# Kernel optimization log

Hardware: AMD Instinct MI355X
Metric: run time of the kernel (lower is better)

The kernel has to match this reference:

```python
import jax, jax.numpy as jnp
import numpy as np
from jax import lax

FILTER_SIZE = 3
C_IN = 128
C_OUT = 256
PAD = 1
STRIDE = 1


def setup_inputs() -> dict:
    key = jax.random.key(0)
    k1, k2 = jax.random.split(key)
    prev_a = jax.random.normal(k1, (32, 56, 56, C_IN), dtype=jnp.float32)
    # filter_w initialized ~ N(0, 1) as in the original tf.random.normal
    filter_w = jax.random.normal(k2, (FILTER_SIZE, FILTER_SIZE, C_IN, C_OUT), dtype=jnp.float32)
    filter_b = jnp.zeros((1, 1, 1, C_OUT), dtype=jnp.float32)
    return {"prev_a": prev_a, "filter_w": filter_w, "filter_b": filter_b}


def reference(prev_a, filter_w, filter_b):
    # NHWC input, HWIO filter -> NHWC output; same math as the nested-loop conv:
    # z[i,h,w,c] = sum(prev_a_pad[i, h*s:h*s+f, w*s:w*s+f, :] * W[:,:,:,c]) + b[c]
    z = lax.conv_general_dilated(
        prev_a,
        filter_w,
        window_strides=(STRIDE, STRIDE),
        padding=[(PAD, PAD), (PAD, PAD)],
        dimension_numbers=("NHWC", "HWIO", "NHWC"),
    )
    z = z + filter_b  # bias broadcast over (m, H, W)
    return jax.nn.relu(z)
```

## Files before the change

### kernel.cpp

```cpp
#include <hip/hip_runtime.h>
#include <hip/hip_bf16.h>


#define NIMG 32
#define HH 56
#define WW 56
#define PH 58
#define PW 58
#define CIN 128
#define COUT 256
#define KTOT 1152
#define PAD_ELEMS (NIMG * PH * PW * CIN)

typedef __attribute__((ext_vector_type(8))) short bf16x8;
typedef __attribute__((ext_vector_type(4))) short s16x4;
typedef __attribute__((ext_vector_type(4))) float f32x4;

__device__ __forceinline__ short f2bf(float x) {
    union { __hip_bfloat16 b; short s; } u;
    u.b = __float2bfloat16(x);
    return u.s;
}

typedef const void __attribute__((address_space(1)))* gas1_t;
typedef void __attribute__((address_space(3)))* las3_t;
__device__ __forceinline__ void async16(short* lds, const short* g) {
    __builtin_amdgcn_global_load_lds((gas1_t)g, (las3_t)lds, 16, 0, 0);
}

__global__ __launch_bounds__(256) void pack_input(const float* __restrict__ in,
                                                  short* __restrict__ pad) {
    const int tid  = blockIdx.x * 256 + threadIdx.x;
    const int flat = tid * 8;
    const int c8   = flat & (CIN - 1);
    const int rest = flat >> 7;
    const int iw   = rest % PW;
    const int r2   = rest / PW;
    const int ih   = r2 % PH;
    const int img  = r2 / PH;
    bf16x8 v = (bf16x8)0;
    if (ih >= 1 && ih <= HH && iw >= 1 && iw <= WW) {
        const float* p = in + (((size_t)(img * HH + ih - 1) * WW + (iw - 1)) * CIN + c8);
        const float4 x0 = *(const float4*)p;
        const float4 x1 = *(const float4*)(p + 4);
        v.s0 = f2bf(x0.x); v.s1 = f2bf(x0.y); v.s2 = f2bf(x0.z); v.s3 = f2bf(x0.w);
        v.s4 = f2bf(x1.x); v.s5 = f2bf(x1.y); v.s6 = f2bf(x1.z); v.s7 = f2bf(x1.w);
    }
    *(bf16x8*)(pad + flat) = v;
}

__global__ __launch_bounds__(256) void pack_wgt(const float* __restrict__ w,
                                                short* __restrict__ wt) {
    __shared__ short tile[32][33];
    const int k0 = blockIdx.x * 32;
    const int n0 = blockIdx.y * 32;
    const int t  = threadIdx.x;
    {
        const int kl  = t >> 3;
        const int nl4 = (t & 7) * 4;
        const float4 x = *(const float4*)(w + (size_t)(k0 + kl) * COUT + n0 + nl4);
        tile[kl][nl4 + 0] = f2bf(x.x);
        tile[kl][nl4 + 1] = f2bf(x.y);
        tile[kl][nl4 + 2] = f2bf(x.z);
        tile[kl][nl4 + 3] = f2bf(x.w);
    }
    __syncthreads();
    {
        const int nl  = t >> 3;
        const int kl4 = (t & 7) * 4;
        s16x4 v;
        v.x = tile[kl4 + 0][nl];
        v.y = tile[kl4 + 1][nl];
        v.z = tile[kl4 + 2][nl];
        v.w = tile[kl4 + 3][nl];
        *(s16x4*)(wt + (size_t)(n0 + nl) * KTOT + k0 + kl4) = v;
    }
}

__global__ __launch_bounds__(256) void conv_mfma(const short* __restrict__ apad,
                                                 const short* __restrict__ bwt,
                                                 const float* __restrict__ bias,
                                                 float* __restrict__ out) {
    __shared__ short As[128 * 32];
    __shared__ short Bs[128 * 32];

    const int t  = threadIdx.x;
    const int l  = t & 63;
    const int w  = t >> 6;
    const int m0 = blockIdx.y * 128;
    const int n0 = blockIdx.x * 128;

    const int kchunk = t & 3;
    const int row0   = t >> 2;
    int abase[2], bbase[2];
#pragma unroll
    for (int j = 0; j < 2; ++j) {
        const int m   = m0 + row0 + j * 64;
        const int img = m / (HH * WW);
        const int rem = m - img * (HH * WW);
        const int oh  = rem / WW;
        const int ow  = rem - oh * WW;
        abase[j] = ((img * PH + oh) * PW + ow) * CIN + kchunk * 8;
        bbase[j] = (n0 + row0 + j * 64) * KTOT + kchunk * 8;
    }

    f32x4 acc[4][4];
#pragma unroll
    for (int i = 0; i < 4; ++i)
#pragma unroll
        for (int j = 0; j < 4; ++j) { f32x4 z = {0.f, 0.f, 0.f, 0.f}; acc[i][j] = z; }

    const int wm = w & 1;
    const int wn = w >> 1;
    const int fr = l & 15;
    const int fq = l >> 4;

    for (int kt = 0; kt < KTOT / 32; ++kt) {
        const int fhw  = kt >> 2;
        const int ci0  = (kt & 3) * 32;
        const int fh   = fhw / 3;
        const int fw   = fhw - fh * 3;
        const int aoff = (fh * PW + fw) * CIN + ci0;
        const int boff = kt * 32;

        __syncthreads();
#pragma unroll
        for (int j = 0; j < 2; ++j) {
            async16(As + (j * 256 + w * 64) * 8, apad + abase[j] + aoff);
            async16(Bs + (j * 256 + w * 64) * 8, bwt + bbase[j] + boff);
        }
        __syncthreads();

        bf16x8 af[4], bf[4];
#pragma unroll
        for (int i = 0; i < 4; ++i)
            af[i] = *(bf16x8*)&As[(wm * 64 + i * 16 + fr) * 32 + fq * 8];
#pragma unroll
        for (int j = 0; j < 4; ++j)
            bf[j] = *(bf16x8*)&Bs[(wn * 64 + j * 16 + fr) * 32 + fq * 8];
#pragma unroll
        for (int i = 0; i < 4; ++i)
#pragma unroll
            for (int j = 0; j < 4; ++j)
                acc[i][j] = __builtin_amdgcn_mfma_f32_16x16x32_bf16(af[i], bf[j], acc[i][j], 0, 0, 0);
    }

#pragma unroll
    for (int j = 0; j < 4; ++j) {
        const int n  = n0 + wn * 64 + j * 16 + fr;
        const float bj = bias[n];
#pragma unroll
        for (int i = 0; i < 4; ++i) {
            const int mrow = m0 + wm * 64 + i * 16 + fq * 4;
#pragma unroll
            for (int r = 0; r < 4; ++r) {
                const float v = acc[i][j][r] + bj;
                out[(size_t)(mrow + r) * COUT + n] = v > 0.f ? v : 0.f;
            }
        }
    }
}

extern "C" void kernel_launch(void* const* d_in, const int* in_sizes, int n_in,
                              void* d_out, int out_size, void* d_ws, size_t ws_size,
                              hipStream_t stream) {
    const float* in   = (const float*)d_in[0];
    const float* wgt  = (const float*)d_in[1];
    const float* bias = (const float*)d_in[2];
    float* out = (float*)d_out;

    short* pad = (short*)d_ws;
    short* wt  = (short*)d_ws + PAD_ELEMS;

    pack_input<<<PAD_ELEMS / 8 / 256, 256, 0, stream>>>(in, pad);
    pack_wgt<<<dim3(KTOT / 32, COUT / 32), 256, 0, stream>>>(wgt, wt);

    dim3 grid(COUT / 128, (NIMG * HH * WW) / 128);
    conv_mfma<<<grid, 256, 0, stream>>>(pad, wt, bias, out);
}
```

Before: 224.1 us.

## Double-buffer LDS tiles and XOR-swizzle the layout in the conv MFMA kernel

```diff
diff --git a/kernel.cpp b/kernel.cpp
--- a/kernel.cpp
+++ b/kernel.cpp
@@ -11,6 +11,9 @@
 #define COUT 256
 #define KTOT 1152
 #define PAD_ELEMS (NIMG * PH * PW * CIN)
+
+#define BK 32
+#define KITERS (KTOT / BK)
 
 typedef __attribute__((ext_vector_type(8))) short bf16x8;
 typedef __attribute__((ext_vector_type(4))) short s16x4;
@@ -81,8 +84,8 @@
                                                  const short* __restrict__ bwt,
                                                  const float* __restrict__ bias,
                                                  float* __restrict__ out) {
-    __shared__ short As[128 * 32];
-    __shared__ short Bs[128 * 32];
+    __shared__ short As0[128 * BK], As1[128 * BK];
+    __shared__ short Bs0[128 * BK], Bs1[128 * BK];
 
     const int t  = threadIdx.x;
     const int l  = t & 63;
@@ -90,18 +93,19 @@
     const int m0 = blockIdx.y * 128;
     const int n0 = blockIdx.x * 128;
 
-    const int kchunk = t & 3;
-    const int row0   = t >> 2;
+    const int Lc = (t & 7) ^ ((t >> 3) & 7);
+    const int kc = Lc & 3;
     int abase[2], bbase[2];
 #pragma unroll
     for (int j = 0; j < 2; ++j) {
-        const int m   = m0 + row0 + j * 64;
+        const int r   = 2 * (t >> 3) + (Lc >> 2) + j * 64;
+        const int m   = m0 + r;
         const int img = m / (HH * WW);
         const int rem = m - img * (HH * WW);
         const int oh  = rem / WW;
         const int ow  = rem - oh * WW;
-        abase[j] = ((img * PH + oh) * PW + ow) * CIN + kchunk * 8;
-        bbase[j] = (n0 + row0 + j * 64) * KTOT + kchunk * 8;
+        abase[j] = ((img * PH + oh) * PW + ow) * CIN + kc * 8;
+        bbase[j] = (n0 + r) * KTOT + kc * 8;
     }
 
     f32x4 acc[4][4];
@@ -115,34 +119,45 @@
     const int fr = l & 15;
     const int fq = l >> 4;
 
-    for (int kt = 0; kt < KTOT / 32; ++kt) {
-        const int fhw  = kt >> 2;
-        const int ci0  = (kt & 3) * 32;
-        const int fh   = fhw / 3;
-        const int fw   = fhw - fh * 3;
-        const int aoff = (fh * PW + fw) * CIN + ci0;
-        const int boff = kt * 32;
+#define STAGE(KT, AS, BS) do {                                              \
+        const int _fhw  = (KT) >> 2;                                        \
+        const int _fh   = _fhw / 3;                                         \
+        const int _fw   = _fhw - _fh * 3;                                   \
+        const int _aoff = (_fh * PW + _fw) * CIN + ((KT) & 3) * 32;         \
+        const int _boff = (KT) * BK;                                        \
+        _Pragma("unroll")                                                   \
+        for (int _j = 0; _j < 2; ++_j) {                                    \
+            async16((AS) + (_j * 256 + w * 64) * 8, apad + abase[_j] + _aoff); \
+            async16((BS) + (_j * 256 + w * 64) * 8, bwt + bbase[_j] + _boff); \
+        }                                                                   \
+    } while (0)
 
+#define FRAG(BASE, R) \
+    (*(const bf16x8*)((BASE) + (((R) >> 1) << 6) + \
+     (((((R) & 1) << 2) | fq) ^ (((R) >> 1) & 7)) * 8))
+
+#define COMPUTE(AS, BS) do {                                                \
+        bf16x8 _af[4], _bf[4];                                              \
+        _Pragma("unroll")                                                   \
+        for (int _i = 0; _i < 4; ++_i) _af[_i] = FRAG(AS, wm * 64 + _i * 16 + fr); \
+        _Pragma("unroll")                                                   \
+        for (int _j = 0; _j < 4; ++_j) _bf[_j] = FRAG(BS, wn * 64 + _j * 16 + fr); \
+        _Pragma("unroll")                                                   \
+        for (int _i = 0; _i < 4; ++_i)                                      \
+            _Pragma("unroll")                                               \
+            for (int _j = 0; _j < 4; ++_j)                                  \
+                acc[_i][_j] = __builtin_amdgcn_mfma_f32_16x16x32_bf16(      \
+                    _af[_i], _bf[_j], acc[_i][_j], 0, 0, 0);                \
+    } while (0)
+
+    STAGE(0, As0, Bs0);
+    for (int kt = 0; kt < KITERS; kt += 2) {
         __syncthreads();
-#pragma unroll
-        for (int j = 0; j < 2; ++j) {
-            async16(As + (j * 256 + w * 64) * 8, apad + abase[j] + aoff);
-            async16(Bs + (j * 256 + w * 64) * 8, bwt + bbase[j] + boff);
-        }
+        STAGE(kt + 1, As1, Bs1);
+        COMPUTE(As0, Bs0);
         __syncthreads();
-
-        bf16x8 af[4], bf[4];
-#pragma unroll
-        for (int i = 0; i < 4; ++i)
-            af[i] = *(bf16x8*)&As[(wm * 64 + i * 16 + fr) * 32 + fq * 8];
-#pragma unroll
-        for (int j = 0; j < 4; ++j)
-            bf[j] = *(bf16x8*)&Bs[(wn * 64 + j * 16 + fr) * 32 + fq * 8];
-#pragma unroll
-        for (int i = 0; i < 4; ++i)
-#pragma unroll
-            for (int j = 0; j < 4; ++j)
-                acc[i][j] = __builtin_amdgcn_mfma_f32_16x16x32_bf16(af[i], bf[j], acc[i][j], 0, 0, 0);
+        if (kt + 2 < KITERS) STAGE(kt + 2, As0, Bs0);
+        COMPUTE(As1, Bs1);
     }
 
 #pragma unroll
@@ -159,6 +174,9 @@
             }
         }
     }
+#undef STAGE
+#undef FRAG
+#undef COMPUTE
 }
 
 extern "C" void kernel_launch(void* const* d_in, const int* in_sizes, int n_in,
```

After: 221.7 us. Within noise of the previous version (-1.1%).

## Load MFMA fragments directly from global with register prefetch, dropping LDS staging

Applied to the files above, without the earlier changes.

```diff
diff --git a/kernel.cpp b/kernel.cpp
--- a/kernel.cpp
+++ b/kernel.cpp
@@ -11,6 +11,7 @@
 #define COUT 256
 #define KTOT 1152
 #define PAD_ELEMS (NIMG * PH * PW * CIN)
+#define KITERS 36
 
 typedef __attribute__((ext_vector_type(8))) short bf16x8;
 typedef __attribute__((ext_vector_type(4))) short s16x4;
@@ -20,12 +21,6 @@
     union { __hip_bfloat16 b; short s; } u;
     u.b = __float2bfloat16(x);
     return u.s;
-}
-
-typedef const void __attribute__((address_space(1)))* gas1_t;
-typedef void __attribute__((address_space(3)))* las3_t;
-__device__ __forceinline__ void async16(short* lds, const short* g) {
-    __builtin_amdgcn_global_load_lds((gas1_t)g, (las3_t)lds, 16, 0, 0);
 }
 
 __global__ __launch_bounds__(256) void pack_input(const float* __restrict__ in,
@@ -77,32 +72,35 @@
     }
 }
 
-__global__ __launch_bounds__(256) void conv_mfma(const short* __restrict__ apad,
-                                                 const short* __restrict__ bwt,
-                                                 const float* __restrict__ bias,
-                                                 float* __restrict__ out) {
-    __shared__ short As[128 * 32];
-    __shared__ short Bs[128 * 32];
-
+__global__ __launch_bounds__(256, 2) void conv_mfma(const short* __restrict__ apad,
+                                                    const short* __restrict__ bwt,
+                                                    const float* __restrict__ bias,
+                                                    float* __restrict__ out) {
     const int t  = threadIdx.x;
     const int l  = t & 63;
     const int w  = t >> 6;
     const int m0 = blockIdx.y * 128;
     const int n0 = blockIdx.x * 128;
 
-    const int kchunk = t & 3;
-    const int row0   = t >> 2;
-    int abase[2], bbase[2];
+    const int wm = w & 1;
+    const int wn = w >> 1;
+    const int fr = l & 15;
+    const int fq = l >> 4;
+
+    const short* abase[4];
 #pragma unroll
-    for (int j = 0; j < 2; ++j) {
-        const int m   = m0 + row0 + j * 64;
+    for (int i = 0; i < 4; ++i) {
+        const int m   = m0 + wm * 64 + i * 16 + fr;
         const int img = m / (HH * WW);
         const int rem = m - img * (HH * WW);
         const int oh  = rem / WW;
         const int ow  = rem - oh * WW;
-        abase[j] = ((img * PH + oh) * PW + ow) * CIN + kchunk * 8;
-        bbase[j] = (n0 + row0 + j * 64) * KTOT + kchunk * 8;
+        abase[i] = apad + ((img * PH + oh) * PW + ow) * CIN + fq * 8;
     }
+    const short* bbase[4];
+#pragma unroll
+    for (int j = 0; j < 4; ++j)
+        bbase[j] = bwt + (n0 + wn * 64 + j * 16 + fr) * KTOT + fq * 8;
 
     f32x4 acc[4][4];
 #pragma unroll
@@ -110,40 +108,37 @@
 #pragma unroll
         for (int j = 0; j < 4; ++j) { f32x4 z = {0.f, 0.f, 0.f, 0.f}; acc[i][j] = z; }
 
-    const int wm = w & 1;
-    const int wn = w >> 1;
-    const int fr = l & 15;
-    const int fq = l >> 4;
+#define AOFF(KT) ((((KT) >> 2) / 3 * PW + (((KT) >> 2) % 3)) * CIN + ((KT) & 3) * 32)
+#define BOFF(KT) ((KT) * 32)
 
-    for (int kt = 0; kt < KTOT / 32; ++kt) {
-        const int fhw  = kt >> 2;
-        const int ci0  = (kt & 3) * 32;
-        const int fh   = fhw / 3;
-        const int fw   = fhw - fh * 3;
-        const int aoff = (fh * PW + fw) * CIN + ci0;
-        const int boff = kt * 32;
+    bf16x8 ac[4], bc[4];
+#pragma unroll
+    for (int i = 0; i < 4; ++i) ac[i] = *(const bf16x8*)(abase[i] + AOFF(0));
+#pragma unroll
+    for (int j = 0; j < 4; ++j) bc[j] = *(const bf16x8*)(bbase[j] + BOFF(0));
 
-        __syncthreads();
 #pragma unroll
-        for (int j = 0; j < 2; ++j) {
-            async16(As + (j * 256 + w * 64) * 8, apad + abase[j] + aoff);
-            async16(Bs + (j * 256 + w * 64) * 8, bwt + bbase[j] + boff);
+    for (int kt = 0; kt < KITERS; ++kt) {
+        bf16x8 an[4], bn[4];
+        if (kt + 1 < KITERS) {
+            const int ao = AOFF(kt + 1), bo = BOFF(kt + 1);
+#pragma unroll
+            for (int i = 0; i < 4; ++i) an[i] = *(const bf16x8*)(abase[i] + ao);
+#pragma unroll
+            for (int j = 0; j < 4; ++j) bn[j] = *(const bf16x8*)(bbase[j] + bo);
         }
-        __syncthreads();
-
-        bf16x8 af[4], bf[4];
-#pragma unroll
-        for (int i = 0; i < 4; ++i)
-            af[i] = *(bf16x8*)&As[(wm * 64 + i * 16 + fr) * 32 + fq * 8];
-#pragma unroll
-        for (int j = 0; j < 4; ++j)
-            bf[j] = *(bf16x8*)&Bs[(wn * 64 + j * 16 + fr) * 32 + fq * 8];
 #pragma unroll
         for (int i = 0; i < 4; ++i)
 #pragma unroll
             for (int j = 0; j < 4; ++j)
-                acc[i][j] = __builtin_amdgcn_mfma_f32_16x16x32_bf16(af[i], bf[j], acc[i][j], 0, 0, 0);
+                acc[i][j] = __builtin_amdgcn_mfma_f32_16x16x32_bf16(ac[i], bc[j], acc[i][j], 0, 0, 0);
+        if (kt + 1 < KITERS) {
+#pragma unroll
+            for (int i = 0; i < 4; ++i) { ac[i] = an[i]; bc[i] = bn[i]; }
+        }
     }
+#undef AOFF
+#undef BOFF
 
 #pragma unroll
     for (int j = 0; j < 4; ++j) {
```

Result: slower. 371.2 us (+65.6%).
